# Kernel optimization log

Hardware: AMD Instinct MI355X
Metric: run time of the kernel (lower is better)

The kernel has to match this reference:

```python
import jax, jax.numpy as jnp
import numpy as np

BATCH, IN, HID, NCLS = 4096, 2048, 8192, 1000

def setup_inputs() -> dict:
    key = jax.random.key(0)
    kx, kk, kg = jax.random.split(key, 3)
    x = jax.random.normal(kx, (BATCH, IN), dtype=jnp.float32)
    # torch nn.Linear weights: kohonen [HID, IN], grossberg [NCLS, HID], init U(-1, 1)
    Wk = jax.random.uniform(kk, (HID, IN), dtype=jnp.float32, minval=-1.0, maxval=1.0)
    Wg = jax.random.uniform(kg, (NCLS, HID), dtype=jnp.float32, minval=-1.0, maxval=1.0)
    return {"x": x, "Wk": Wk, "Wg": Wg}

def reference(x, Wk, Wg):
    # L2-normalize each row
    xn = x / jnp.linalg.norm(x, axis=1, keepdims=True)  # [B, IN]
    kohonen_out = jnp.einsum('bi,hi->bh', xn, Wk)        # [B, HID]
    idx = jnp.argmax(kohonen_out, axis=1)                # [B] winner units
    # one-hot @ Wg.T == gather columns of Wg for winning units
    out = jnp.take(Wg, idx, axis=1).T                    # [B, NCLS]
    return out
```

## Files before the change

### kernel.cpp

```cpp
#include <hip/hip_runtime.h>
#include <stdint.h>

typedef unsigned int u32;
typedef unsigned long long u64;
typedef unsigned short u16;
typedef unsigned char u8;
typedef int intx8 __attribute__((ext_vector_type(8)));
typedef float floatx4 __attribute__((ext_vector_type(4)));

#define BATCH 4096
#define IN    2048
#define HID   8192
#define NCLS  1000

#define OFF_ROWKEY 0u
#define OFF_TOPK   32768u
#define OFF_X8     8421376u
#define OFF_WK8    16809984u
#define OFF_WGT    33587200u
#define TOTAL_FULL 66355200ull

__device__ __forceinline__ u32 fkey(float f) {
    u32 u = __float_as_uint(f);
    return (u & 0x80000000u) ? ~u : (u | 0x80000000u);
}
__device__ __forceinline__ float unfkey(u32 k) {
    return __uint_as_float((k & 0x80000000u) ? (k ^ 0x80000000u) : ~k);
}
__device__ __forceinline__ void ce32(u32& a, u32& b) {
    u32 mx = a > b ? a : b;
    u32 mn = a > b ? b : a;
    a = mx; b = mn;
}

__global__ __launch_bounds__(256) void prep_kernel(
    const float* __restrict__ x, const float* __restrict__ Wk,
    const float* __restrict__ Wg,
    u8* __restrict__ x8, u8* __restrict__ wk8, float* __restrict__ WgT)
{
    __shared__ float t[32][33];
    const int bid = blockIdx.x;
    if (bid < 1024) {
        const int gid = bid * 256 + threadIdx.x;
        const int NSX = BATCH * IN / 16;
        const int NS  = NSX + HID * IN / 16;
        for (int s = gid; s < NS; s += 1024 * 256) {
            const float4* src; u8* dst;
            if (s < NSX) { src = (const float4*)x + (size_t)s * 4;  dst = x8  + (size_t)s * 16; }
            else { int u = s - NSX; src = (const float4*)Wk + (size_t)u * 4; dst = wk8 + (size_t)u * 16; }
            uint4 o;
            float4 f;
            int p;
            f = src[0];
            p = __builtin_amdgcn_cvt_pk_fp8_f32(f.x, f.y, 0, false);
            p = __builtin_amdgcn_cvt_pk_fp8_f32(f.z, f.w, p, true);  o.x = (u32)p;
            f = src[1];
            p = __builtin_amdgcn_cvt_pk_fp8_f32(f.x, f.y, 0, false);
            p = __builtin_amdgcn_cvt_pk_fp8_f32(f.z, f.w, p, true);  o.y = (u32)p;
            f = src[2];
            p = __builtin_amdgcn_cvt_pk_fp8_f32(f.x, f.y, 0, false);
            p = __builtin_amdgcn_cvt_pk_fp8_f32(f.z, f.w, p, true);  o.z = (u32)p;
            f = src[3];
            p = __builtin_amdgcn_cvt_pk_fp8_f32(f.x, f.y, 0, false);
            p = __builtin_amdgcn_cvt_pk_fp8_f32(f.z, f.w, p, true);  o.w = (u32)p;
            *(uint4*)dst = o;
        }
    } else {
        const int tb = bid - 1024;
        const int bx = (tb & 255) * 32;
        const int by = (tb >> 8) * 32;
        const int tx = threadIdx.x & 31, ty = threadIdx.x >> 5;
        #pragma unroll
        for (int i = 0; i < 32; i += 8) {
            int c = by + ty + i;
            t[ty + i][tx] = (c < NCLS) ? Wg[(size_t)c * HID + bx + tx] : 0.f;
        }
        __syncthreads();
        #pragma unroll
        for (int i = 0; i < 32; i += 8) {
            int c = by + tx;
            if (c < NCLS) WgT[(size_t)(bx + ty + i) * NCLS + by + tx] = t[tx][ty + i];
        }
    }
}

#define STAGE(gsrc, ldsoff) \
    __builtin_amdgcn_global_load_lds((const __attribute__((address_space(1))) u32*)(gsrc), \
        (__attribute__((address_space(3))) u32*)&LDS[ldsoff], 16, 0, 0)

__global__ __launch_bounds__(512) void mfma_fp8_gemm_kernel(
    const u8* __restrict__ x8, const u8* __restrict__ wk8,
    u32* __restrict__ topk)
{
    __shared__ __align__(16) u8 LDS[3 * 49152];

    const int tid  = threadIdx.x;
    const int lane = tid & 63;
    const int w    = tid >> 6;
    const int bm   = blockIdx.y * 128;
    const int bn   = blockIdx.x * 256;
    const int wrow = (w >> 2) * 64;
    const int wcol = (w & 3) * 64;
    const int m = lane & 15, q = lane >> 4;

    floatx4 acc[4][4];
    #pragma unroll
    for (int i = 0; i < 4; i++)
        #pragma unroll
        for (int j = 0; j < 4; j++)
            acc[i][j] = (floatx4){0.f, 0.f, 0.f, 0.f};

    const int srow = tid >> 3;
    const int soff = (((((tid >> 1) & 3) ^ (srow & 3)) * 2) + (tid & 1)) * 16;
    const u8* gxa = x8  + (size_t)(bm + srow) * IN + soff;
    const u8* gwb = wk8 + (size_t)(bn + srow) * IN + soff;
    const u32 ldst = (u32)tid * 16;

    const int foq  = (q ^ (m & 3)) * 32;
    const u32 aoff = (u32)(wrow + m) * 128 + (u32)foq;
    const u32 boff = 16384u + (u32)(wcol + m) * 128 + (u32)foq;

    STAGE(gxa,                            0u         + ldst);
    STAGE(gxa +  64 * (size_t)IN,         8192u      + ldst);
    STAGE(gwb,                            16384u     + ldst);
    STAGE(gwb +  64 * (size_t)IN,         24576u     + ldst);
    STAGE(gwb + 128 * (size_t)IN,         32768u     + ldst);
    STAGE(gwb + 192 * (size_t)IN,         40960u     + ldst);
    __builtin_amdgcn_sched_barrier(0);
    STAGE(gxa + 128,                      49152u          + ldst);
    STAGE(gxa +  64 * (size_t)IN + 128,   49152u + 8192u  + ldst);
    STAGE(gwb + 128,                      49152u + 16384u + ldst);
    STAGE(gwb +  64 * (size_t)IN + 128,   49152u + 24576u + ldst);
    STAGE(gwb + 128 * (size_t)IN + 128,   49152u + 32768u + ldst);
    STAGE(gwb + 192 * (size_t)IN + 128,   49152u + 40960u + ldst);
    asm volatile("s_waitcnt vmcnt(6)" ::: "memory");
    __builtin_amdgcn_s_barrier();

    u32 rb = 0u;
    u32 sb = 98304u;

    #pragma unroll 1
    for (int kt = 0; kt < 16; ++kt) {
        const size_t ko2 = (size_t)(kt + 2) * 128;
        intx8 af[4];
        #pragma unroll
        for (int i = 0; i < 4; i++)
            af[i] = *(const intx8*)&LDS[rb + aoff + (u32)i * 2048u];
        intx8 bf0 = *(const intx8*)&LDS[rb + boff];
        intx8 bf1 = *(const intx8*)&LDS[rb + boff + 2048u];
        if (kt < 14) {
            STAGE(gxa + ko2,                      sb          + ldst);
            STAGE(gxa +  64 * (size_t)IN + ko2,   sb + 8192u  + ldst);
            STAGE(gwb + ko2,                      sb + 16384u + ldst);
        }
        asm volatile("" ::: "memory");
        __builtin_amdgcn_s_barrier();
        asm volatile("s_waitcnt lgkmcnt(0)" ::: "memory");
        __builtin_amdgcn_sched_barrier(0);
        __builtin_amdgcn_s_setprio(1);
        #pragma unroll
        for (int i = 0; i < 4; i++)
            acc[i][0] = __builtin_amdgcn_mfma_scale_f32_16x16x128_f8f6f4(
                af[i], bf0, acc[i][0], 0, 0, 0, 0x7F, 0, 0x7F);
        #pragma unroll
        for (int i = 0; i < 4; i++)
            acc[i][1] = __builtin_amdgcn_mfma_scale_f32_16x16x128_f8f6f4(
                af[i], bf1, acc[i][1], 0, 0, 0, 0x7F, 0, 0x7F);
        __builtin_amdgcn_s_setprio(0);
        asm volatile("" ::: "memory");
        __builtin_amdgcn_s_barrier();
        intx8 bf2 = *(const intx8*)&LDS[rb + boff + 4096u];
        intx8 bf3 = *(const intx8*)&LDS[rb + boff + 6144u];
        if (kt < 14) {
            STAGE(gwb +  64 * (size_t)IN + ko2,   sb + 24576u + ldst);
            STAGE(gwb + 128 * (size_t)IN + ko2,   sb + 32768u + ldst);
            STAGE(gwb + 192 * (size_t)IN + ko2,   sb + 40960u + ldst);
        }
        asm volatile("" ::: "memory");
        __builtin_amdgcn_s_barrier();
        asm volatile("s_waitcnt lgkmcnt(0)" ::: "memory");
        __builtin_amdgcn_sched_barrier(0);
        __builtin_amdgcn_s_setprio(1);
        #pragma unroll
        for (int i = 0; i < 4; i++)
            acc[i][2] = __builtin_amdgcn_mfma_scale_f32_16x16x128_f8f6f4(
                af[i], bf2, acc[i][2], 0, 0, 0, 0x7F, 0, 0x7F);
        #pragma unroll
        for (int i = 0; i < 4; i++)
            acc[i][3] = __builtin_amdgcn_mfma_scale_f32_16x16x128_f8f6f4(
                af[i], bf3, acc[i][3], 0, 0, 0, 0x7F, 0, 0x7F);
        __builtin_amdgcn_s_setprio(0);
        if (kt < 13)       asm volatile("s_waitcnt vmcnt(6)" ::: "memory");
        else               asm volatile("s_waitcnt vmcnt(0)" ::: "memory");
        __builtin_amdgcn_s_barrier();
        rb = (rb == 98304u) ? 0u : rb + 49152u;
        sb = (sb == 98304u) ? 0u : sb + 49152u;
    }

    const int group = blockIdx.x * 4 + (w & 3);
    #pragma unroll
    for (int i = 0; i < 4; i++) {
        #pragma unroll
        for (int r = 0; r < 4; r++) {
            u32 k0 = (fkey(acc[i][0][r]) & 0xFFFFFFC0u) | (0u << 4) | (u32)m;
            u32 k1 = (fkey(acc[i][1][r]) & 0xFFFFFFC0u) | (1u << 4) | (u32)m;
            u32 k2 = (fkey(acc[i][2][r]) & 0xFFFFFFC0u) | (2u << 4) | (u32)m;
            u32 k3 = (fkey(acc[i][3][r]) & 0xFFFFFFC0u) | (3u << 4) | (u32)m;
            ce32(k0, k1); ce32(k2, k3); ce32(k0, k2); ce32(k1, k3); ce32(k1, k2);
            #pragma unroll
            for (int off = 1; off < 16; off <<= 1) {
                u32 b0 = __shfl_xor(k0, off, 64);
                u32 b1 = __shfl_xor(k1, off, 64);
                u32 b2 = __shfl_xor(k2, off, 64);
                u32 b3 = __shfl_xor(k3, off, 64);
                u32 t0 = k0 > b3 ? k0 : b3;
                u32 t1 = k1 > b2 ? k1 : b2;
                u32 t2 = k2 > b1 ? k2 : b1;
                u32 t3 = k3 > b0 ? k3 : b0;
                ce32(t0, t2); ce32(t1, t3); ce32(t0, t1); ce32(t2, t3);
                k0 = t0; k1 = t1; k2 = t2; k3 = t3;
            }
            if (m == 0) {
                const int grow = bm + wrow + i * 16 + q * 4 + r;
                uint4 v; v.x = k0; v.y = k1; v.z = k2; v.w = k3;
                *(uint4*)&topk[(size_t)grow * 512 + group * 4] = v;
            }
        }
    }
}

__global__ __launch_bounds__(256) void scan_kernel(
    const u32* __restrict__ topk,
    const float* __restrict__ x, const float* __restrict__ Wk,
    const float* __restrict__ WgT, float* __restrict__ out)
{
    __shared__ u16 cand[4][48];
    const int wv   = threadIdx.x >> 6;
    const int lane = threadIdx.x & 63;
    const int row  = blockIdx.x * 4 + wv;

    const uint4* tp = (const uint4*)(topk + (size_t)row * 512);
    uint4 v0 = tp[lane];
    uint4 v1 = tp[lane + 64];

    u32 mx = v0.x > v1.x ? v0.x : v1.x;
    #pragma unroll
    for (int off = 1; off < 64; off <<= 1) {
        u32 o = __shfl_xor(mx, off, 64);
        if (o > mx) mx = o;
    }
    const float thr = unfkey(mx & 0xFFFFFFC0u) - 12.0f;

    int base = 0;
    const u32 ks[8] = {v0.x, v0.y, v0.z, v0.w, v1.x, v1.y, v1.z, v1.w};
    #pragma unroll
    for (int s = 0; s < 8; s++) {
        const int group = (s < 4) ? lane : (lane + 64);
        const u32 key = ks[s];
        const bool in = unfkey(key & 0xFFFFFFC0u) >= thr;
        const u64 msk = __ballot(in);
        if (in) {
            int rnk = base + __popcll(msk & ((1ull << lane) - 1ull));
            if (rnk < 48)
                cand[wv][rnk] = (u16)(group * 64 + (int)((key >> 4) & 3u) * 16 + (int)(key & 15u));
        }
        base += __popcll(msk);
    }
    const int n = min(base, 48);
    __builtin_amdgcn_wave_barrier();

    int col;
    if (n <= 1) {
        col = cand[wv][0];
    } else {
        const float4* xr = (const float4*)(x + (size_t)row * IN);
        float4 a[8];
        #pragma unroll
        for (int p = 0; p < 8; p++) a[p] = xr[p * 64 + lane];
        u64 best = 0ull;
        for (int c = 0; c < n; c++) {
            const int h = cand[wv][c];
            const float4* wr = (const float4*)(Wk + (size_t)h * IN);
            float s = 0.f;
            #pragma unroll
            for (int p = 0; p < 8; p++) {
                float4 b = wr[p * 64 + lane];
                s += a[p].x * b.x + a[p].y * b.y + a[p].z * b.z + a[p].w * b.w;
            }
            #pragma unroll
            for (int off = 1; off < 64; off <<= 1) s += __shfl_xor(s, off, 64);
            u64 key = ((u64)fkey(s) << 32) | (u64)(0x1FFFu - (u32)h);
            if (key > best) best = key;
        }
        col = 0x1FFF - (int)(best & 0xFFFFu);
    }

    const float4* src = (const float4*)(WgT + (size_t)col * NCLS);
    float4* dst = (float4*)(out + (size_t)row * NCLS);
    for (int t = lane; t < NCLS / 4; t += 64) dst[t] = src[t];
}

__global__ void init_ws_kernel(u64* rowkey) {
    int i = blockIdx.x * blockDim.x + threadIdx.x;
    if (i < BATCH) rowkey[i] = 0ULL;
}

__global__ __launch_bounds__(256) void gemm_argmax_kernel(
    const float* __restrict__ x, const float* __restrict__ Wk,
    u64* __restrict__ rowkey)
{
    __shared__ __align__(16) float As[32 * 64];
    __shared__ __align__(16) float Bs[32 * 64];
    const int tid = threadIdx.x;
    const int bm = blockIdx.y * 64, bn = blockIdx.x * 64;
    const int tx = tid & 15, ty = tid >> 4;
    float acc[4][4];
    #pragma unroll
    for (int i = 0; i < 4; i++)
        #pragma unroll
        for (int j = 0; j < 4; j++) acc[i][j] = 0.f;
    const int r0 = tid >> 3, q0 = tid & 7;
    const int r1 = (tid + 256) >> 3, q1 = (tid + 256) & 7;
    const float* xA0 = &x[(size_t)(bm + r0) * IN + q0 * 4];
    const float* xA1 = &x[(size_t)(bm + r1) * IN + q1 * 4];
    const float* wB0 = &Wk[(size_t)(bn + r0) * IN + q0 * 4];
    const float* wB1 = &Wk[(size_t)(bn + r1) * IN + q1 * 4];
    for (int k0 = 0; k0 < IN; k0 += 32) {
        float4 a0 = *(const float4*)(xA0 + k0);
        float4 a1 = *(const float4*)(xA1 + k0);
        float4 b0 = *(const float4*)(wB0 + k0);
        float4 b1 = *(const float4*)(wB1 + k0);
        __syncthreads();
        As[(q0 * 4 + 0) * 64 + r0] = a0.x; As[(q0 * 4 + 1) * 64 + r0] = a0.y;
        As[(q0 * 4 + 2) * 64 + r0] = a0.z; As[(q0 * 4 + 3) * 64 + r0] = a0.w;
        As[(q1 * 4 + 0) * 64 + r1] = a1.x; As[(q1 * 4 + 1) * 64 + r1] = a1.y;
        As[(q1 * 4 + 2) * 64 + r1] = a1.z; As[(q1 * 4 + 3) * 64 + r1] = a1.w;
        Bs[(q0 * 4 + 0) * 64 + r0] = b0.x; Bs[(q0 * 4 + 1) * 64 + r0] = b0.y;
        Bs[(q0 * 4 + 2) * 64 + r0] = b0.z; Bs[(q0 * 4 + 3) * 64 + r0] = b0.w;
        Bs[(q1 * 4 + 0) * 64 + r1] = b1.x; Bs[(q1 * 4 + 1) * 64 + r1] = b1.y;
        Bs[(q1 * 4 + 2) * 64 + r1] = b1.z; Bs[(q1 * 4 + 3) * 64 + r1] = b1.w;
        __syncthreads();
        #pragma unroll
        for (int k = 0; k < 32; k++) {
            float4 av = *(const float4*)&As[k * 64 + ty * 4];
            float4 bv = *(const float4*)&Bs[k * 64 + tx * 4];
            acc[0][0] += av.x * bv.x; acc[0][1] += av.x * bv.y;
            acc[0][2] += av.x * bv.z; acc[0][3] += av.x * bv.w;
            acc[1][0] += av.y * bv.x; acc[1][1] += av.y * bv.y;
            acc[1][2] += av.y * bv.z; acc[1][3] += av.y * bv.w;
            acc[2][0] += av.z * bv.x; acc[2][1] += av.z * bv.y;
            acc[2][2] += av.z * bv.z; acc[2][3] += av.z * bv.w;
            acc[3][0] += av.w * bv.x; acc[3][1] += av.w * bv.y;
            acc[3][2] += av.w * bv.z; acc[3][3] += av.w * bv.w;
        }
    }
    #pragma unroll
    for (int i = 0; i < 4; i++) {
        const int row = bm + ty * 4 + i;
        u64 best = 0ULL;
        #pragma unroll
        for (int j = 0; j < 4; j++) {
            const int col = bn + tx * 4 + j;
            u64 p = ((u64)fkey(acc[i][j]) << 32) | (u64)(0x1FFFu - (unsigned)col);
            if (p > best) best = p;
        }
        #pragma unroll
        for (int off = 1; off < 16; off <<= 1) {
            u64 other = __shfl_xor(best, off, 64);
            if (other > best) best = other;
        }
        if (tx == 0) atomicMax(&rowkey[row], best);
    }
}

__global__ __launch_bounds__(256) void gather_kernel(
    const u64* __restrict__ rowkey, const float* __restrict__ Wg,
    float* __restrict__ out)
{
    const int b = blockIdx.y;
    const int c = blockIdx.x * 256 + threadIdx.x;
    if (c >= NCLS) return;
    const int col = 0x1FFF - (int)(rowkey[b] & 0xFFFFFFFFu);
    out[(size_t)b * NCLS + c] = Wg[(size_t)c * HID + col];
}

extern "C" void kernel_launch(void* const* d_in, const int* in_sizes, int n_in,
                              void* d_out, int out_size, void* d_ws, size_t ws_size,
                              hipStream_t stream) {
    const float* x  = (const float*)d_in[0];
    const float* Wk = (const float*)d_in[1];
    const float* Wg = (const float*)d_in[2];
    float* out = (float*)d_out;
    char* ws = (char*)d_ws;

    if (ws_size >= TOTAL_FULL) {
        u32* topk  = (u32*)(ws + OFF_TOPK);
        u8*  x8    = (u8*)(ws + OFF_X8);
        u8*  wk8   = (u8*)(ws + OFF_WK8);
        float* WgT = (float*)(ws + OFF_WGT);

        hipLaunchKernelGGL(prep_kernel, dim3(1024 + 8192), dim3(256), 0, stream,
                           x, Wk, Wg, x8, wk8, WgT);
        hipLaunchKernelGGL(mfma_fp8_gemm_kernel, dim3(HID / 256, BATCH / 128), dim3(512), 0, stream,
                           x8, wk8, topk);
        hipLaunchKernelGGL(scan_kernel, dim3(BATCH / 4), dim3(256), 0, stream,
                           topk, x, Wk, WgT, out);
    } else {
        u64* rowkey = (u64*)(ws + OFF_ROWKEY);
        hipLaunchKernelGGL(init_ws_kernel, dim3(16), dim3(256), 0, stream, rowkey);
        hipLaunchKernelGGL(gemm_argmax_kernel, dim3(HID / 64, BATCH / 64), dim3(256), 0, stream,
                           x, Wk, rowkey);
        hipLaunchKernelGGL(gather_kernel, dim3(4, BATCH), dim3(256), 0, stream,
                           rowkey, Wg, out);
    }
}
```

Before: 323.8 us.

## Register double-buffer MFMA fragments and unroll k-loop with one barrier per tile

Rewrites the fp8 GEMM main loop as a fully unrolled loop that prefetches the next k-tile's A/B fragments from LDS into a second register set while MFMAs run on the current set. All six global-to-LDS stages for tile k+2 are issued at the start of each iteration, and the per-iteration barrier count drops from three to one. The LDS swizzle becomes an 8-way XOR over 16-byte granules, and each fragment is read as two 16-byte loads to reduce bank conflicts. The cost is doubled fragment registers, which may lower occupancy or cause spills. The end-of-iteration vmcnt(0) wait also shortens the effective global prefetch depth.

```diff
diff --git a/kernel.cpp b/kernel.cpp
--- a/kernel.cpp
+++ b/kernel.cpp
@@ -5,6 +5,7 @@
 typedef unsigned long long u64;
 typedef unsigned short u16;
 typedef unsigned char u8;
+typedef int intx4 __attribute__((ext_vector_type(4)));
 typedef int intx8 __attribute__((ext_vector_type(8)));
 typedef float floatx4 __attribute__((ext_vector_type(4)));
 
@@ -88,6 +89,63 @@
     __builtin_amdgcn_global_load_lds((const __attribute__((address_space(1))) u32*)(gsrc), \
         (__attribute__((address_space(3))) u32*)&LDS[ldsoff], 16, 0, 0)
 
+#define RD_A(dst, base) { _Pragma("unroll") for (int i_ = 0; i_ < 4; i_++) { \
+    intx4 lo_ = *(const intx4*)&LDS[(base) + aAddr[i_] + sLo]; \
+    intx4 hi_ = *(const intx4*)&LDS[(base) + aAddr[i_] + sHi]; \
+    dst[i_] = __builtin_shufflevector(lo_, hi_, 0,1,2,3,4,5,6,7); } }
+
+#define RD_B01(dst, base) { _Pragma("unroll") for (int j_ = 0; j_ < 2; j_++) { \
+    intx4 lo_ = *(const intx4*)&LDS[(base) + bAddr[j_] + sLo]; \
+    intx4 hi_ = *(const intx4*)&LDS[(base) + bAddr[j_] + sHi]; \
+    dst[j_] = __builtin_shufflevector(lo_, hi_, 0,1,2,3,4,5,6,7); } }
+
+#define RD_B23(dst, base) { _Pragma("unroll") for (int j_ = 2; j_ < 4; j_++) { \
+    intx4 lo_ = *(const intx4*)&LDS[(base) + bAddr[j_] + sLo]; \
+    intx4 hi_ = *(const intx4*)&LDS[(base) + bAddr[j_] + sHi]; \
+    dst[j_] = __builtin_shufflevector(lo_, hi_, 0,1,2,3,4,5,6,7); } }
+
+#define MFMA_J(afX, bfX, J) { _Pragma("unroll") for (int i_ = 0; i_ < 4; i_++) \
+    acc[i_][J] = __builtin_amdgcn_mfma_scale_f32_16x16x128_f8f6f4( \
+        afX[i_], bfX[J], acc[i_][J], 0, 0, 0, 0x7F, 0, 0x7F); }
+
+#define KT_BODY(KT, afC, bfC, afN, bfN)                                        \
+{                                                                              \
+    const u32 nb_   = (u32)(((KT) + 1) % 3) * 49152u;                          \
+    const u32 sbuf_ = (u32)(((KT) + 2) % 3) * 49152u;                          \
+    if ((KT) < 14) {                                                           \
+        const size_t ko_ = (size_t)((KT) + 2) * 128;                           \
+        STAGE(gxa + ko_,                     sbuf_          + ldst);           \
+        STAGE(gxa +  64 * (size_t)IN + ko_,  sbuf_ + 8192u  + ldst);           \
+        STAGE(gwb + ko_,                     sbuf_ + 16384u + ldst);           \
+        STAGE(gwb +  64 * (size_t)IN + ko_,  sbuf_ + 24576u + ldst);           \
+        STAGE(gwb + 128 * (size_t)IN + ko_,  sbuf_ + 32768u + ldst);           \
+        STAGE(gwb + 192 * (size_t)IN + ko_,  sbuf_ + 40960u + ldst);           \
+    }                                                                          \
+    asm volatile("s_waitcnt lgkmcnt(4)" ::: "memory");       \
+    __builtin_amdgcn_sched_barrier(0);                                         \
+    if ((KT) < 15) { RD_A(afN, nb_) }                          \
+    asm volatile("" ::: "memory");                                             \
+    __builtin_amdgcn_s_setprio(1);                                             \
+    MFMA_J(afC, bfC, 0)                                                        \
+    MFMA_J(afC, bfC, 1)                                                        \
+    __builtin_amdgcn_s_setprio(0);                                             \
+    if ((KT) < 15) { asm volatile("s_waitcnt lgkmcnt(8)" ::: "memory"); }      \
+    else           { asm volatile("s_waitcnt lgkmcnt(0)" ::: "memory"); }      \
+    __builtin_amdgcn_sched_barrier(0);                                         \
+    if ((KT) < 15) { RD_B01(bfN, nb_) }                        \
+    asm volatile("" ::: "memory");                                             \
+    __builtin_amdgcn_s_setprio(1);                                             \
+    MFMA_J(afC, bfC, 2)                                                        \
+    MFMA_J(afC, bfC, 3)                                                        \
+    __builtin_amdgcn_s_setprio(0);                                             \
+    if ((KT) < 15) { RD_B23(bfN, nb_) }                        \
+    if ((KT) < 15) {                                                           \
+        asm volatile("s_waitcnt vmcnt(0)" ::: "memory");      \
+        __builtin_amdgcn_s_barrier();                                          \
+        asm volatile("" ::: "memory");                                         \
+    }                                                                          \
+}
+
 __global__ __launch_bounds__(512) void mfma_fp8_gemm_kernel(
     const u8* __restrict__ x8, const u8* __restrict__ wk8,
     u32* __restrict__ topk)
@@ -111,14 +169,20 @@
             acc[i][j] = (floatx4){0.f, 0.f, 0.f, 0.f};
 
     const int srow = tid >> 3;
-    const int soff = (((((tid >> 1) & 3) ^ (srow & 3)) * 2) + (tid & 1)) * 16;
+    const int soff = ((tid & 7) ^ (srow & 7)) * 16;
     const u8* gxa = x8  + (size_t)(bm + srow) * IN + soff;
     const u8* gwb = wk8 + (size_t)(bn + srow) * IN + soff;
     const u32 ldst = (u32)tid * 16;
 
-    const int foq  = (q ^ (m & 3)) * 32;
-    const u32 aoff = (u32)(wrow + m) * 128 + (u32)foq;
-    const u32 boff = 16384u + (u32)(wcol + m) * 128 + (u32)foq;
+    const u32 sLo = ((((u32)q << 1) ^ ((u32)m & 7u))) * 16u;
+    const u32 sHi = sLo ^ 16u;
+    u32 aAddr[4], bAddr[4];
+    #pragma unroll
+    for (int i = 0; i < 4; i++) aAddr[i] = (u32)(wrow + i * 16 + m) * 128u;
+    #pragma unroll
+    for (int j = 0; j < 4; j++) bAddr[j] = 16384u + (u32)(wcol + j * 16 + m) * 128u;
+
+    intx8 afA[4], bfA[4], afB[4], bfB[4];
 
     STAGE(gxa,                            0u         + ldst);
     STAGE(gxa +  64 * (size_t)IN,         8192u      + ldst);
@@ -126,75 +190,26 @@
     STAGE(gwb +  64 * (size_t)IN,         24576u     + ldst);
     STAGE(gwb + 128 * (size_t)IN,         32768u     + ldst);
     STAGE(gwb + 192 * (size_t)IN,         40960u     + ldst);
-    __builtin_amdgcn_sched_barrier(0);
     STAGE(gxa + 128,                      49152u          + ldst);
     STAGE(gxa +  64 * (size_t)IN + 128,   49152u + 8192u  + ldst);
     STAGE(gwb + 128,                      49152u + 16384u + ldst);
     STAGE(gwb +  64 * (size_t)IN + 128,   49152u + 24576u + ldst);
     STAGE(gwb + 128 * (size_t)IN + 128,   49152u + 32768u + ldst);
     STAGE(gwb + 192 * (size_t)IN + 128,   49152u + 40960u + ldst);
-    asm volatile("s_waitcnt vmcnt(6)" ::: "memory");
+    asm volatile("s_waitcnt vmcnt(0)" ::: "memory");
     __builtin_amdgcn_s_barrier();
-
-    u32 rb = 0u;
-    u32 sb = 98304u;
-
-    #pragma unroll 1
-    for (int kt = 0; kt < 16; ++kt) {
-        const size_t ko2 = (size_t)(kt + 2) * 128;
-        intx8 af[4];
-        #pragma unroll
-        for (int i = 0; i < 4; i++)
-            af[i] = *(const intx8*)&LDS[rb + aoff + (u32)i * 2048u];
-        intx8 bf0 = *(const intx8*)&LDS[rb + boff];
-        intx8 bf1 = *(const intx8*)&LDS[rb + boff + 2048u];
-        if (kt < 14) {
-            STAGE(gxa + ko2,                      sb          + ldst);
-            STAGE(gxa +  64 * (size_t)IN + ko2,   sb + 8192u  + ldst);
-            STAGE(gwb + ko2,                      sb + 16384u + ldst);
-        }
-        asm volatile("" ::: "memory");
-        __builtin_amdgcn_s_barrier();
-        asm volatile("s_waitcnt lgkmcnt(0)" ::: "memory");
-        __builtin_amdgcn_sched_barrier(0);
-        __builtin_amdgcn_s_setprio(1);
-        #pragma unroll
-        for (int i = 0; i < 4; i++)
-            acc[i][0] = __builtin_amdgcn_mfma_scale_f32_16x16x128_f8f6f4(
-                af[i], bf0, acc[i][0], 0, 0, 0, 0x7F, 0, 0x7F);
-        #pragma unroll
-        for (int i = 0; i < 4; i++)
-            acc[i][1] = __builtin_amdgcn_mfma_scale_f32_16x16x128_f8f6f4(
-                af[i], bf1, acc[i][1], 0, 0, 0, 0x7F, 0, 0x7F);
-        __builtin_amdgcn_s_setprio(0);
-        asm volatile("" ::: "memory");
-        __builtin_amdgcn_s_barrier();
-        intx8 bf2 = *(const intx8*)&LDS[rb + boff + 4096u];
-        intx8 bf3 = *(const intx8*)&LDS[rb + boff + 6144u];
-        if (kt < 14) {
-            STAGE(gwb +  64 * (size_t)IN + ko2,   sb + 24576u + ldst);
-            STAGE(gwb + 128 * (size_t)IN + ko2,   sb + 32768u + ldst);
-            STAGE(gwb + 192 * (size_t)IN + ko2,   sb + 40960u + ldst);
-        }
-        asm volatile("" ::: "memory");
-        __builtin_amdgcn_s_barrier();
-        asm volatile("s_waitcnt lgkmcnt(0)" ::: "memory");
-        __builtin_amdgcn_sched_barrier(0);
-        __builtin_amdgcn_s_setprio(1);
-        #pragma unroll
-        for (int i = 0; i < 4; i++)
-            acc[i][2] = __builtin_amdgcn_mfma_scale_f32_16x16x128_f8f6f4(
-                af[i], bf2, acc[i][2], 0, 0, 0, 0x7F, 0, 0x7F);
-        #pragma unroll
-        for (int i = 0; i < 4; i++)
-            acc[i][3] = __builtin_amdgcn_mfma_scale_f32_16x16x128_f8f6f4(
-                af[i], bf3, acc[i][3], 0, 0, 0, 0x7F, 0, 0x7F);
-        __builtin_amdgcn_s_setprio(0);
-        if (kt < 13)       asm volatile("s_waitcnt vmcnt(6)" ::: "memory");
-        else               asm volatile("s_waitcnt vmcnt(0)" ::: "memory");
-        __builtin_amdgcn_s_barrier();
-        rb = (rb == 98304u) ? 0u : rb + 49152u;
-        sb = (sb == 98304u) ? 0u : sb + 49152u;
+    asm volatile("" ::: "memory");
+    RD_A(afA, 0u)
+    asm volatile("" ::: "memory");
+    RD_B01(bfA, 0u)
+    asm volatile("" ::: "memory");
+    RD_B23(bfA, 0u)
+    asm volatile("" ::: "memory");
+
+    #pragma unroll
+    for (int kp = 0; kp < 8; ++kp) {
+        KT_BODY(kp * 2,     afA, bfA, afB, bfB)
+        KT_BODY(kp * 2 + 1, afB, bfB, afA, bfA)
     }
 
     const int group = blockIdx.x * 4 + (w & 3);
```

Result: slower. 703.4 us (+117.3%).

## Enlarge GEMM block tile to 256x256 with double-buffered LDS pipeline

Applied to the files above, without the earlier changes.

The FP8 MFMA GEMM block tile grows from 128x256 to 256x256, so each wave computes a 128x64 sub-tile with 8x4 accumulators. The LDS ring changes from three 48KB stages to two 64KB stages, with prefetch one K-step ahead, and the staging loads are spread across four compute phases. Each block loads fewer bytes from global memory per output element, and there are half as many blocks. The costs are higher register pressure, only double buffering, fewer blocks to fill the CUs, and a launch bound that requests 2 blocks/CU, which 128KB of LDS per block may not allow.

```diff
diff --git a/kernel.cpp b/kernel.cpp
--- a/kernel.cpp
+++ b/kernel.cpp
@@ -84,28 +84,31 @@
     }
 }
 
-#define STAGE(gsrc, ldsoff) \
+#define STG(gsrc, ldsoff) \
     __builtin_amdgcn_global_load_lds((const __attribute__((address_space(1))) u32*)(gsrc), \
         (__attribute__((address_space(3))) u32*)&LDS[ldsoff], 16, 0, 0)
 
-__global__ __launch_bounds__(512) void mfma_fp8_gemm_kernel(
+#define MFMA1(A_, B_, C_) C_ = __builtin_amdgcn_mfma_scale_f32_16x16x128_f8f6f4( \
+    A_, B_, C_, 0, 0, 0, 0x7F, 0, 0x7F)
+
+__global__ __launch_bounds__(512, 2) void mfma_fp8_gemm_kernel(
     const u8* __restrict__ x8, const u8* __restrict__ wk8,
     u32* __restrict__ topk)
 {
-    __shared__ __align__(16) u8 LDS[3 * 49152];
+    __shared__ __align__(16) u8 LDS[2 * 65536];
 
     const int tid  = threadIdx.x;
     const int lane = tid & 63;
     const int w    = tid >> 6;
-    const int bm   = blockIdx.y * 128;
+    const int bm   = blockIdx.y * 256;
     const int bn   = blockIdx.x * 256;
-    const int wrow = (w >> 2) * 64;
+    const int wrow = (w >> 2) * 128;
     const int wcol = (w & 3) * 64;
     const int m = lane & 15, q = lane >> 4;
 
-    floatx4 acc[4][4];
-    #pragma unroll
-    for (int i = 0; i < 4; i++)
+    floatx4 acc[8][4];
+    #pragma unroll
+    for (int i = 0; i < 8; i++)
         #pragma unroll
         for (int j = 0; j < 4; j++)
             acc[i][j] = (floatx4){0.f, 0.f, 0.f, 0.f};
@@ -116,42 +119,36 @@
     const u8* gwb = wk8 + (size_t)(bn + srow) * IN + soff;
     const u32 ldst = (u32)tid * 16;
 
-    const int foq  = (q ^ (m & 3)) * 32;
-    const u32 aoff = (u32)(wrow + m) * 128 + (u32)foq;
-    const u32 boff = 16384u + (u32)(wcol + m) * 128 + (u32)foq;
-
-    STAGE(gxa,                            0u         + ldst);
-    STAGE(gxa +  64 * (size_t)IN,         8192u      + ldst);
-    STAGE(gwb,                            16384u     + ldst);
-    STAGE(gwb +  64 * (size_t)IN,         24576u     + ldst);
-    STAGE(gwb + 128 * (size_t)IN,         32768u     + ldst);
-    STAGE(gwb + 192 * (size_t)IN,         40960u     + ldst);
-    __builtin_amdgcn_sched_barrier(0);
-    STAGE(gxa + 128,                      49152u          + ldst);
-    STAGE(gxa +  64 * (size_t)IN + 128,   49152u + 8192u  + ldst);
-    STAGE(gwb + 128,                      49152u + 16384u + ldst);
-    STAGE(gwb +  64 * (size_t)IN + 128,   49152u + 24576u + ldst);
-    STAGE(gwb + 128 * (size_t)IN + 128,   49152u + 32768u + ldst);
-    STAGE(gwb + 192 * (size_t)IN + 128,   49152u + 40960u + ldst);
-    asm volatile("s_waitcnt vmcnt(6)" ::: "memory");
+    const u32 foq = (u32)((q ^ (m & 3)) * 32);
+
+    STG(gxa,                      0u     + ldst);
+    STG(gxa + 128 * (size_t)IN,   16384u + ldst);
+    STG(gwb,                      32768u + ldst);
+    STG(gwb +  64 * (size_t)IN,   40960u + ldst);
+    STG(gwb + 128 * (size_t)IN,   49152u + ldst);
+    STG(gwb + 192 * (size_t)IN,   57344u + ldst);
+    STG(gxa +  64 * (size_t)IN,   8192u  + ldst);
+    STG(gxa + 192 * (size_t)IN,   24576u + ldst);
+    asm volatile("s_waitcnt vmcnt(2)" ::: "memory");
     __builtin_amdgcn_s_barrier();
 
-    u32 rb = 0u;
-    u32 sb = 98304u;
+    u32 cb = 0u;
+
+    intx8 af[4], bf[4];
 
     #pragma unroll 1
     for (int kt = 0; kt < 16; ++kt) {
-        const size_t ko2 = (size_t)(kt + 2) * 128;
-        intx8 af[4];
+        const u32 nb = cb ^ 65536u;
+        const size_t ko = (size_t)(kt + 1) * 128;
         #pragma unroll
         for (int i = 0; i < 4; i++)
-            af[i] = *(const intx8*)&LDS[rb + aoff + (u32)i * 2048u];
-        intx8 bf0 = *(const intx8*)&LDS[rb + boff];
-        intx8 bf1 = *(const intx8*)&LDS[rb + boff + 2048u];
-        if (kt < 14) {
-            STAGE(gxa + ko2,                      sb          + ldst);
-            STAGE(gxa +  64 * (size_t)IN + ko2,   sb + 8192u  + ldst);
-            STAGE(gwb + ko2,                      sb + 16384u + ldst);
+            af[i] = *(const intx8*)&LDS[cb + (u32)(wrow + i * 16 + m) * 128u + foq];
+        #pragma unroll
+        for (int j = 0; j < 2; j++)
+            bf[j] = *(const intx8*)&LDS[cb + 32768u + (u32)(wcol + j * 16 + m) * 128u + foq];
+        if (kt < 15) {
+            STG(gxa + ko,                     nb + ldst);
+            STG(gxa + 128 * (size_t)IN + ko,  nb + 16384u + ldst);
         }
         asm volatile("" ::: "memory");
         __builtin_amdgcn_s_barrier();
@@ -159,22 +156,18 @@
         __builtin_amdgcn_sched_barrier(0);
         __builtin_amdgcn_s_setprio(1);
         #pragma unroll
-        for (int i = 0; i < 4; i++)
-            acc[i][0] = __builtin_amdgcn_mfma_scale_f32_16x16x128_f8f6f4(
-                af[i], bf0, acc[i][0], 0, 0, 0, 0x7F, 0, 0x7F);
-        #pragma unroll
-        for (int i = 0; i < 4; i++)
-            acc[i][1] = __builtin_amdgcn_mfma_scale_f32_16x16x128_f8f6f4(
-                af[i], bf1, acc[i][1], 0, 0, 0, 0x7F, 0, 0x7F);
+        for (int i = 0; i < 4; i++) { MFMA1(af[i], bf[0], acc[i][0]); }
+        #pragma unroll
+        for (int i = 0; i < 4; i++) { MFMA1(af[i], bf[1], acc[i][1]); }
         __builtin_amdgcn_s_setprio(0);
         asm volatile("" ::: "memory");
         __builtin_amdgcn_s_barrier();
-        intx8 bf2 = *(const intx8*)&LDS[rb + boff + 4096u];
-        intx8 bf3 = *(const intx8*)&LDS[rb + boff + 6144u];
-        if (kt < 14) {
-            STAGE(gwb +  64 * (size_t)IN + ko2,   sb + 24576u + ldst);
-            STAGE(gwb + 128 * (size_t)IN + ko2,   sb + 32768u + ldst);
-            STAGE(gwb + 192 * (size_t)IN + ko2,   sb + 40960u + ldst);
+        #pragma unroll
+        for (int j = 2; j < 4; j++)
+            bf[j] = *(const intx8*)&LDS[cb + 32768u + (u32)(wcol + j * 16 + m) * 128u + foq];
+        if (kt < 15) {
+            STG(gwb + ko,                     nb + 32768u + ldst);
+            STG(gwb +  64 * (size_t)IN + ko,  nb + 40960u + ldst);
         }
         asm volatile("" ::: "memory");
         __builtin_amdgcn_s_barrier();
@@ -182,24 +175,52 @@
         __builtin_amdgcn_sched_barrier(0);
         __builtin_amdgcn_s_setprio(1);
         #pragma unroll
+        for (int i = 0; i < 4; i++) { MFMA1(af[i], bf[2], acc[i][2]); }
+        #pragma unroll
+        for (int i = 0; i < 4; i++) { MFMA1(af[i], bf[3], acc[i][3]); }
+        __builtin_amdgcn_s_setprio(0);
+        if (kt < 15) asm volatile("s_waitcnt vmcnt(4)" ::: "memory");
+        else         asm volatile("s_waitcnt vmcnt(0)" ::: "memory");
+        __builtin_amdgcn_s_barrier();
+        #pragma unroll
         for (int i = 0; i < 4; i++)
-            acc[i][2] = __builtin_amdgcn_mfma_scale_f32_16x16x128_f8f6f4(
-                af[i], bf2, acc[i][2], 0, 0, 0, 0x7F, 0, 0x7F);
-        #pragma unroll
-        for (int i = 0; i < 4; i++)
-            acc[i][3] = __builtin_amdgcn_mfma_scale_f32_16x16x128_f8f6f4(
-                af[i], bf3, acc[i][3], 0, 0, 0, 0x7F, 0, 0x7F);
+            af[i] = *(const intx8*)&LDS[cb + (u32)(wrow + 64 + i * 16 + m) * 128u + foq];
+        if (kt < 15) {
+            STG(gwb + 128 * (size_t)IN + ko,  nb + 49152u + ldst);
+            STG(gwb + 192 * (size_t)IN + ko,  nb + 57344u + ldst);
+        }
+        asm volatile("" ::: "memory");
+        __builtin_amdgcn_s_barrier();
+        asm volatile("s_waitcnt lgkmcnt(0)" ::: "memory");
+        __builtin_amdgcn_sched_barrier(0);
+        __builtin_amdgcn_s_setprio(1);
+        #pragma unroll
+        for (int i = 0; i < 4; i++) { MFMA1(af[i], bf[0], acc[4 + i][0]); }
+        #pragma unroll
+        for (int i = 0; i < 4; i++) { MFMA1(af[i], bf[1], acc[4 + i][1]); }
         __builtin_amdgcn_s_setprio(0);
-        if (kt < 13)       asm volatile("s_waitcnt vmcnt(6)" ::: "memory");
-        else               asm volatile("s_waitcnt vmcnt(0)" ::: "memory");
-        __builtin_amdgcn_s_barrier();
-        rb = (rb == 98304u) ? 0u : rb + 49152u;
-        sb = (sb == 98304u) ? 0u : sb + 49152u;
+        asm volatile("" ::: "memory");
+        __builtin_amdgcn_s_barrier();
+        if (kt < 15) {
+            STG(gxa +  64 * (size_t)IN + ko,  nb + 8192u  + ldst);
+            STG(gxa + 192 * (size_t)IN + ko,  nb + 24576u + ldst);
+        }
+        asm volatile("" ::: "memory");
+        __builtin_amdgcn_s_barrier();
+        __builtin_amdgcn_s_setprio(1);
+        #pragma unroll
+        for (int i = 0; i < 4; i++) { MFMA1(af[i], bf[2], acc[4 + i][2]); }
+        #pragma unroll
+        for (int i = 0; i < 4; i++) { MFMA1(af[i], bf[3], acc[4 + i][3]); }
+        __builtin_amdgcn_s_setprio(0);
+        if (kt < 15) asm volatile("s_waitcnt vmcnt(2)" ::: "memory");
+        __builtin_amdgcn_s_barrier();
+        cb = nb;
     }
 
     const int group = blockIdx.x * 4 + (w & 3);
     #pragma unroll
-    for (int i = 0; i < 4; i++) {
+    for (int i = 0; i < 8; i++) {
         #pragma unroll
         for (int r = 0; r < 4; r++) {
             u32 k0 = (fkey(acc[i][0][r]) & 0xFFFFFFC0u) | (0u << 4) | (u32)m;
@@ -401,7 +422,7 @@
 
         hipLaunchKernelGGL(prep_kernel, dim3(1024 + 8192), dim3(256), 0, stream,
                            x, Wk, Wg, x8, wk8, WgT);
-        hipLaunchKernelGGL(mfma_fp8_gemm_kernel, dim3(HID / 256, BATCH / 128), dim3(512), 0, stream,
+        hipLaunchKernelGGL(mfma_fp8_gemm_kernel, dim3(HID / 256, BATCH / 256), dim3(512), 0, stream,
                            x8, wk8, topk);
         hipLaunchKernelGGL(scan_kernel, dim3(BATCH / 4), dim3(256), 0, stream,
                            topk, x, Wk, WgT, out);
```

After: 318.1 us. No clear change (-1.7%).
